# Optimization experiments

Measured on AMD Instinct MI355X. Metric: run time of the kernel, lower is better.

Reference implementation:

```python
import jax, jax.numpy as jnp
import numpy as np

BN_EPS = 1e-5


def setup_inputs() -> dict:
    key = jax.random.key(0)
    ks = jax.random.split(key, 6)
    B, C, N, K, T, O = 8, 64, 4096, 20, 3, 64
    feat = jax.random.normal(ks[0], (B, C, N), dtype=jnp.float32)
    idx = jax.random.randint(ks[1], (B, N, K), 0, N, dtype=jnp.int32)
    group_pc = jax.random.normal(ks[2], (B, 3, N, K), dtype=jnp.float32)
    weights = jax.random.normal(ks[3], (B, 20, T, N, K), dtype=jnp.float32) * 0.05
    conv_w = jax.random.normal(ks[4], (O, C * T, K), dtype=jnp.float32) * 0.02
    gamma = jnp.ones((O,), dtype=jnp.float32)
    beta = jnp.zeros((O,), dtype=jnp.float32)
    return {"feat": feat, "idx": idx, "group_pc": group_pc, "weights": weights,
            "conv_w": conv_w, "gamma": gamma, "beta": beta}


def _poly_terms(group_pc):
    # group_pc: (B, 3, N, K) -> 20 Taylor terms (B, 20, N, K)
    X, Y, Z = group_pc[:, 0], group_pc[:, 1], group_pc[:, 2]
    XX, YY, ZZ = X * X, Y * Y, Z * Z
    XY, XZ, YZ = X * Y, X * Z, Y * Z
    ones = jnp.ones_like(X)
    return jnp.stack([
        ones, X, Y, Z,
        XX, YY, ZZ,
        XX * X, YY * Y, ZZ * Z,
        XY, XZ, YZ,
        X * XY, X * XZ, Y * YZ, Y * XY, Z * XZ, Z * YZ, XY * Z,
    ], axis=1)


def reference(feat, idx, group_pc, weights, conv_w, gamma, beta):
    B, C, N = feat.shape
    K = idx.shape[-1]
    T = weights.shape[2]
    # KNN gather: group_feat[b, c, n, j] = feat[b, c, idx[b, n, j]]  -> (B, C, N, K)
    group_feat = jax.vmap(lambda f, i: f[:, i])(feat, idx)
    # 20 polynomial basis terms of XYZ: (B, 20, N, K)
    terms = _poly_terms(group_pc)
    # taylor[b, t, n, k] = sum_p weights[b, p, t, n, k] * terms[b, p, n, k]
    taylor = jnp.einsum('bptnk,bpnk->btnk', weights, terms)
    # Fused outer-product + [1, K] conv (output width 1, no bias since bn=True):
    # out[b, o, n] = sum_{c, t, k} group_feat[b,c,n,k] * taylor[b,t,n,k] * W[o, c*T+t, k]
    w = conv_w.reshape(conv_w.shape[0], C, T, K)
    out = jnp.einsum('bcnk,btnk,octk->bon', group_feat, taylor, w)
    # BatchNorm (training-mode batch stats over B and N) + ReLU
    mean = jnp.mean(out, axis=(0, 2), keepdims=True)
    var = jnp.var(out, axis=(0, 2), keepdims=True)
    out = gamma[None, :, None] * (out - mean) / jnp.sqrt(var + BN_EPS) + beta[None, :, None]
    return jax.nn.relu(out)
```

## Files before the change

kernel.cpp:

```cpp
#include <hip/hip_runtime.h>
#include <hip/hip_bf16.h>

#define B_ 8
#define C_ 64
#define N_ 4096
#define K_ 20
#define T_ 3
#define O_ 64
#define P_ 20
#define NK_ (N_ * K_)
#define BN_EPS 1e-5f
#define PADW 68

#define WS_FEATT 0
#define WS_WT (WS_FEATT + B_ * N_ * C_)
#define WS_TAY (WS_WT + 122880)
#define WS_RAW (WS_TAY + B_ * T_ * NK_)
#define WS_PART (WS_RAW + B_ * O_ * N_)
#define WS_STATS (WS_PART + 512 * O_ * 2)

typedef __attribute__((ext_vector_type(8))) short short8;
typedef __attribute__((ext_vector_type(16))) float f32x16;

__device__ inline unsigned cvtpk_bf16(float lo, float hi) {
    unsigned r;
    asm volatile("v_cvt_pk_bf16_f32 %0, %1, %2" : "=v"(r) : "v"(lo), "v"(hi));
    return r;
}

union U128 {
    uint4 u;
    short8 s;
};
__device__ inline short8 as_short8(uint4 u) {
    U128 x;
    x.u = u;
    return x.s;
}

__global__ void k_transpose_feat(const float* __restrict__ feat, float* __restrict__ featT) {
    __shared__ float t[64][65];
    int b = blockIdx.y;
    int n0 = blockIdx.x * 64;
    int lx = threadIdx.x & 63, ly = threadIdx.x >> 6;
    const float* fp = feat + b * C_ * N_;
#pragma unroll
    for (int cc = 0; cc < 16; ++cc) {
        int c = ly * 16 + cc;
        t[c][lx] = fp[c * N_ + n0 + lx];
    }
    __syncthreads();
    float* op = featT + (b * N_ + n0) * C_;
#pragma unroll
    for (int u = 0; u < 16; ++u) {
        int n = ly * 16 + u;
        op[n * C_ + lx] = t[lx][n];
    }
}

__global__ void k_pack_w(const float* __restrict__ cw, unsigned short* __restrict__ Wf) {
    int e = blockIdx.x * 256 + threadIdx.x;
    int j = e & 7;
    int l = (e >> 3) & 63;
    int frag = e >> 9;
    int oh = frag & 1;
    int cc = (frag >> 1) & 3;
    int kt = frag >> 3;
    int t = kt % 3, k = kt / 3;
    int o = oh * 32 + (l & 31);
    int c = cc * 16 + (l >> 5) * 8 + j;
    float v = cw[o * (C_ * T_ * K_) + (c * T_ + t) * K_ + k];
    Wf[e] = (unsigned short)(cvtpk_bf16(v, v) & 0xffffu);
}

__global__ void k_taylor(const float* __restrict__ W5, const float* __restrict__ gpc,
                         float* __restrict__ tay) {
    int tid = blockIdx.x * 256 + threadIdx.x;
    int b = tid / NK_;
    int nk = tid - b * NK_;
    const float X = gpc[b * 3 * NK_ + nk];
    const float Y = gpc[b * 3 * NK_ + NK_ + nk];
    const float Z = gpc[b * 3 * NK_ + 2 * NK_ + nk];
    float XX = X * X, YY = Y * Y, ZZ = Z * Z;
    float XY = X * Y, XZ = X * Z, YZ = Y * Z;
    float terms[20];
    terms[0] = 1.f; terms[1] = X;      terms[2] = Y;       terms[3] = Z;
    terms[4] = XX;  terms[5] = YY;     terms[6] = ZZ;
    terms[7] = XX * X; terms[8] = YY * Y; terms[9] = ZZ * Z;
    terms[10] = XY; terms[11] = XZ;    terms[12] = YZ;
    terms[13] = X * XY;
    terms[14] = X * XZ;
    terms[15] = Y * YZ;
    terms[16] = Y * XY;
    terms[17] = Z * XZ;
    terms[18] = Z * YZ;
    terms[19] = XY * Z;
    float a0 = 0.f, a1 = 0.f, a2 = 0.f;
    const float* wp = W5 + (size_t)b * P_ * T_ * NK_ + nk;
#pragma unroll
    for (int p = 0; p < P_; ++p) {
        float tp = terms[p];
        a0 += wp[0] * tp;
        a1 += wp[NK_] * tp;
        a2 += wp[2 * NK_] * tp;
        wp += 3 * NK_;
    }
    float* tp = tay + (size_t)b * T_ * NK_ + nk;
    tp[0] = a0;
    tp[NK_] = a1;
    tp[2 * NK_] = a2;
}

__global__ __launch_bounds__(512, 4) void k_main(const float* __restrict__ featT,
                                                 const unsigned short* __restrict__ Wf,
                                                 const float* __restrict__ tay,
                                                 const int* __restrict__ idx,
                                                 float* __restrict__ raw,
                                                 float* __restrict__ part) {
    __shared__ float G[2][64][PADW];
    __shared__ union {
        struct {
            float tayS[3][K_][64];
            int idxS[K_][64];
        } s;
        float out[64][68];
    } su;

    const int bid0 = blockIdx.x;
    const int bid = (bid0 & 7) * 64 + (bid0 >> 3);
    const int b = bid >> 6;
    const int n0 = (bid & 63) << 6;
    const int tid = threadIdx.x;
    const int lane = tid & 63;
    const int wv = tid >> 6;
    const int wc = wv & 3;
    const int wo = wv >> 2;
    const int nl = lane & 31;
    const int kf = lane >> 5;

    {
        const int* ip = idx + (b * N_ + n0) * K_;
        for (int e = tid; e < 64 * K_; e += 512) su.s.idxS[e % K_][e / K_] = ip[e];
#pragma unroll
        for (int t = 0; t < 3; ++t) {
            const float* tp = tay + ((size_t)(b * 3 + t) * N_ + n0) * K_;
            for (int e = tid; e < 64 * K_; e += 512) su.s.tayS[t][e % K_][e / K_] = tp[e];
        }
    }
    __syncthreads();

    f32x16 acc[2];
#pragma unroll
    for (int nh = 0; nh < 2; ++nh)
#pragma unroll
        for (int i = 0; i < 16; ++i) acc[nh][i] = 0.f;

    const float* fb = featT + (size_t)b * N_ * C_;
    const int r1 = tid >> 4, r2 = r1 + 32, sseg = tid & 15;

    float4 st1 = *(const float4*)(fb + su.s.idxS[0][r1] * C_ + sseg * 4);
    float4 st2 = *(const float4*)(fb + su.s.idxS[0][r2] * C_ + sseg * 4);

    for (int k = 0; k < K_; ++k) {
        float* Gb = &G[k & 1][0][0];
        *(float4*)(Gb + r1 * PADW + sseg * 4) = st1;
        *(float4*)(Gb + r2 * PADW + sseg * 4) = st2;
        __syncthreads();
        if (k + 1 < K_) {
            st1 = *(const float4*)(fb + su.s.idxS[k + 1][r1] * C_ + sseg * 4);
            st2 = *(const float4*)(fb + su.s.idxS[k + 1][r2] * C_ + sseg * 4);
        }
        const float* row0 = Gb + nl * PADW + wc * 16 + kf * 8;
        const float* row1 = Gb + (nl + 32) * PADW + wc * 16 + kf * 8;
        float4 u0 = *(const float4*)row0, u1 = *(const float4*)(row0 + 4);
        float4 w0 = *(const float4*)row1, w1 = *(const float4*)(row1 + 4);
        float g0[8] = {u0.x, u0.y, u0.z, u0.w, u1.x, u1.y, u1.z, u1.w};
        float g1[8] = {w0.x, w0.y, w0.z, w0.w, w1.x, w1.y, w1.z, w1.w};
#pragma unroll
        for (int t = 0; t < 3; ++t) {
            uint4 ar = *(const uint4*)(Wf +
                                       (size_t)((((k * 3 + t) * 4 + wc) * 2 + wo) * 64 + lane) * 8);
            float tv0 = su.s.tayS[t][k][nl];
            float tv1 = su.s.tayS[t][k][nl + 32];
            unsigned p0[4], p1[4];
#pragma unroll
            for (int p = 0; p < 4; ++p) {
                p0[p] = cvtpk_bf16(g0[2 * p] * tv0, g0[2 * p + 1] * tv0);
                p1[p] = cvtpk_bf16(g1[2 * p] * tv1, g1[2 * p + 1] * tv1);
            }
            short8 bf0 = as_short8(make_uint4(p0[0], p0[1], p0[2], p0[3]));
            short8 bf1 = as_short8(make_uint4(p1[0], p1[1], p1[2], p1[3]));
            short8 a0 = as_short8(ar);
            acc[0] = __builtin_amdgcn_mfma_f32_32x32x16_bf16(a0, bf0, acc[0], 0, 0, 0);
            acc[1] = __builtin_amdgcn_mfma_f32_32x32x16_bf16(a0, bf1, acc[1], 0, 0, 0);
        }
    }

    __syncthreads();
#pragma unroll 1
    for (int ww = 0; ww < 4; ++ww) {
        if (wc == ww) {
#pragma unroll
            for (int nh = 0; nh < 2; ++nh)
#pragma unroll
                for (int r = 0; r < 16; ++r) {
                    int row = wo * 32 + (r & 3) + ((r >> 2) << 3) + (kf << 2);
                    int col = nh * 32 + nl;
                    if (ww == 0)
                        su.out[row][col] = acc[nh][r];
                    else
                        su.out[row][col] += acc[nh][r];
                }
        }
        __syncthreads();
    }

    if (tid < 256) {
        int o = tid >> 2, seg = tid & 3;
        float4* dst = (float4*)(raw + ((b * O_ + o) * N_) + n0 + seg * 16);
        const float* srow = &su.out[o][seg * 16];
        dst[0] = *(const float4*)&srow[0];
        dst[1] = *(const float4*)&srow[4];
        dst[2] = *(const float4*)&srow[8];
        dst[3] = *(const float4*)&srow[12];
    }
    if (tid < 64) {
        float s1 = 0.f, s2 = 0.f;
#pragma unroll 8
        for (int n = 0; n < 64; ++n) {
            float v = su.out[tid][n];
            s1 += v;
            s2 += v * v;
        }
        part[(bid * 64 + tid) * 2 + 0] = s1;
        part[(bid * 64 + tid) * 2 + 1] = s2;
    }
}

__global__ void k_bnstats(const float* __restrict__ part, const float* __restrict__ gamma,
                          const float* __restrict__ beta, float* __restrict__ stats) {
    int o = blockIdx.x;
    int tid = threadIdx.x;
    __shared__ float s1s[256], s2s[256];
    float s1 = 0.f, s2 = 0.f;
    for (int j = tid; j < 512; j += 256) {
        s1 += part[(j * 64 + o) * 2 + 0];
        s2 += part[(j * 64 + o) * 2 + 1];
    }
    s1s[tid] = s1;
    s2s[tid] = s2;
    __syncthreads();
    for (int s = 128; s > 0; s >>= 1) {
        if (tid < s) {
            s1s[tid] += s1s[tid + s];
            s2s[tid] += s2s[tid + s];
        }
        __syncthreads();
    }
    if (tid == 0) {
        const float cnt = (float)(B_ * N_);
        float mean = s1s[0] / cnt;
        float var = s2s[0] / cnt - mean * mean;
        float sc = gamma[o] * rsqrtf(var + BN_EPS);
        stats[o * 2 + 0] = sc;
        stats[o * 2 + 1] = beta[o] - mean * sc;
    }
}

__global__ void k_finalize(const float* __restrict__ raw, const float* __restrict__ stats,
                           float* __restrict__ out) {
    int e = (blockIdx.x * 256 + threadIdx.x) * 4;
    int o = (e >> 12) & 63;
    float sc = stats[o * 2 + 0], sh = stats[o * 2 + 1];
    float4 v = *(const float4*)(raw + e);
    v.x = fmaxf(v.x * sc + sh, 0.f);
    v.y = fmaxf(v.y * sc + sh, 0.f);
    v.z = fmaxf(v.z * sc + sh, 0.f);
    v.w = fmaxf(v.w * sc + sh, 0.f);
    *(float4*)(out + e) = v;
}

extern "C" void kernel_launch(void* const* d_in, const int* in_sizes, int n_in,
                              void* d_out, int out_size, void* d_ws, size_t ws_size,
                              hipStream_t stream) {
    const float* feat = (const float*)d_in[0];
    const int* idx = (const int*)d_in[1];
    const float* gpc = (const float*)d_in[2];
    const float* weights = (const float*)d_in[3];
    const float* conv_w = (const float*)d_in[4];
    const float* gamma = (const float*)d_in[5];
    const float* beta = (const float*)d_in[6];
    float* out = (float*)d_out;
    float* ws = (float*)d_ws;

    float* featT = ws + WS_FEATT;
    unsigned short* Wf = (unsigned short*)(ws + WS_WT);
    float* tay = ws + WS_TAY;
    float* raw = ws + WS_RAW;
    float* part = ws + WS_PART;
    float* stats = ws + WS_STATS;

    hipLaunchKernelGGL(k_transpose_feat, dim3(N_ / 64, B_), dim3(256), 0, stream, feat, featT);
    hipLaunchKernelGGL(k_pack_w, dim3((K_ * T_ * C_ * O_) / 256), dim3(256), 0, stream, conv_w,
                       Wf);
    hipLaunchKernelGGL(k_taylor, dim3(B_ * NK_ / 256), dim3(256), 0, stream, weights, gpc, tay);
    hipLaunchKernelGGL(k_main, dim3(B_ * (N_ / 64)), dim3(512), 0, stream, featT, Wf, tay, idx,
                       raw, part);
    hipLaunchKernelGGL(k_bnstats, dim3(O_), dim3(256), 0, stream, part, gamma, beta, stats);
    hipLaunchKernelGGL(k_finalize, dim3(B_ * O_ * N_ / 4 / 256), dim3(256), 0, stream, raw, stats,
                       out);
}
```

Measured before the change: 83.65 us.

## Fuse Taylor weighting into main kernel and switch MFMA path to fp16

```diff
diff --git a/kernel.cpp b/kernel.cpp
--- a/kernel.cpp
+++ b/kernel.cpp
@@ -14,34 +14,42 @@
 
 #define WS_FEATT 0
 #define WS_WT (WS_FEATT + B_ * N_ * C_)
-#define WS_TAY (WS_WT + 122880)
-#define WS_RAW (WS_TAY + B_ * T_ * NK_)
+#define WS_RAW (WS_WT + 122880)
 #define WS_PART (WS_RAW + B_ * O_ * N_)
 #define WS_STATS (WS_PART + 512 * O_ * 2)
 
-typedef __attribute__((ext_vector_type(8))) short short8;
+typedef __attribute__((ext_vector_type(8))) _Float16 half8;
+typedef __attribute__((ext_vector_type(2))) _Float16 half2v;
+typedef __attribute__((ext_vector_type(2))) __fp16 fp16x2;
 typedef __attribute__((ext_vector_type(16))) float f32x16;
 
-__device__ inline unsigned cvtpk_bf16(float lo, float hi) {
-    unsigned r;
-    asm volatile("v_cvt_pk_bf16_f32 %0, %1, %2" : "=v"(r) : "v"(lo), "v"(hi));
-    return r;
-}
-
-union U128 {
+union UH8 {
     uint4 u;
-    short8 s;
+    half8 h;
+    half2v h2[4];
 };
-__device__ inline short8 as_short8(uint4 u) {
-    U128 x;
-    x.u = u;
-    return x.s;
+union UH2 {
+    unsigned u;
+    half2v h;
+    fp16x2 f;
+};
+
+__device__ inline half2v cvt_pkrtz(float a, float b) {
+    UH2 x;
+    x.f = __builtin_amdgcn_cvt_pkrtz(a, b);
+    return x.h;
+}
+__device__ inline unsigned cvt_pkrtz_u(float a, float b) {
+    UH2 x;
+    x.f = __builtin_amdgcn_cvt_pkrtz(a, b);
+    return x.u;
 }
 
 __global__ void k_transpose_feat(const float* __restrict__ feat, float* __restrict__ featT) {
     __shared__ float t[64][65];
-    int b = blockIdx.y;
-    int n0 = blockIdx.x * 64;
+    int bid = blockIdx.x;
+    int b = bid & 7;
+    int n0 = (bid >> 3) << 6;
     int lx = threadIdx.x & 63, ly = threadIdx.x >> 6;
     const float* fp = feat + b * C_ * N_;
 #pragma unroll
@@ -58,7 +66,7 @@
     }
 }
 
-__global__ void k_pack_w(const float* __restrict__ cw, unsigned short* __restrict__ Wf) {
+__global__ void k_pack_w(const float* __restrict__ cw, _Float16* __restrict__ Wh) {
     int e = blockIdx.x * 256 + threadIdx.x;
     int j = e & 7;
     int l = (e >> 3) & 63;
@@ -69,58 +77,20 @@
     int t = kt % 3, k = kt / 3;
     int o = oh * 32 + (l & 31);
     int c = cc * 16 + (l >> 5) * 8 + j;
-    float v = cw[o * (C_ * T_ * K_) + (c * T_ + t) * K_ + k];
-    Wf[e] = (unsigned short)(cvtpk_bf16(v, v) & 0xffffu);
-}
-
-__global__ void k_taylor(const float* __restrict__ W5, const float* __restrict__ gpc,
-                         float* __restrict__ tay) {
-    int tid = blockIdx.x * 256 + threadIdx.x;
-    int b = tid / NK_;
-    int nk = tid - b * NK_;
-    const float X = gpc[b * 3 * NK_ + nk];
-    const float Y = gpc[b * 3 * NK_ + NK_ + nk];
-    const float Z = gpc[b * 3 * NK_ + 2 * NK_ + nk];
-    float XX = X * X, YY = Y * Y, ZZ = Z * Z;
-    float XY = X * Y, XZ = X * Z, YZ = Y * Z;
-    float terms[20];
-    terms[0] = 1.f; terms[1] = X;      terms[2] = Y;       terms[3] = Z;
-    terms[4] = XX;  terms[5] = YY;     terms[6] = ZZ;
-    terms[7] = XX * X; terms[8] = YY * Y; terms[9] = ZZ * Z;
-    terms[10] = XY; terms[11] = XZ;    terms[12] = YZ;
-    terms[13] = X * XY;
-    terms[14] = X * XZ;
-    terms[15] = Y * YZ;
-    terms[16] = Y * XY;
-    terms[17] = Z * XZ;
-    terms[18] = Z * YZ;
-    terms[19] = XY * Z;
-    float a0 = 0.f, a1 = 0.f, a2 = 0.f;
-    const float* wp = W5 + (size_t)b * P_ * T_ * NK_ + nk;
-#pragma unroll
-    for (int p = 0; p < P_; ++p) {
-        float tp = terms[p];
-        a0 += wp[0] * tp;
-        a1 += wp[NK_] * tp;
-        a2 += wp[2 * NK_] * tp;
-        wp += 3 * NK_;
-    }
-    float* tp = tay + (size_t)b * T_ * NK_ + nk;
-    tp[0] = a0;
-    tp[NK_] = a1;
-    tp[2 * NK_] = a2;
+    Wh[e] = (_Float16)cw[o * (C_ * T_ * K_) + (c * T_ + t) * K_ + k];
 }
 
 __global__ __launch_bounds__(512, 4) void k_main(const float* __restrict__ featT,
-                                                 const unsigned short* __restrict__ Wf,
-                                                 const float* __restrict__ tay,
+                                                 const _Float16* __restrict__ Wh,
+                                                 const float* __restrict__ weights,
+                                                 const float* __restrict__ gpc,
                                                  const int* __restrict__ idx,
                                                  float* __restrict__ raw,
                                                  float* __restrict__ part) {
     __shared__ float G[2][64][PADW];
     __shared__ union {
         struct {
-            float tayS[3][K_][64];
+            unsigned tayH[3][K_][64];
             int idxS[K_][64];
         } s;
         float out[64][68];
@@ -141,10 +111,42 @@
     {
         const int* ip = idx + (b * N_ + n0) * K_;
         for (int e = tid; e < 64 * K_; e += 512) su.s.idxS[e % K_][e / K_] = ip[e];
-#pragma unroll
-        for (int t = 0; t < 3; ++t) {
-            const float* tp = tay + ((size_t)(b * 3 + t) * N_ + n0) * K_;
-            for (int e = tid; e < 64 * K_; e += 512) su.s.tayS[t][e % K_][e / K_] = tp[e];
+    }
+    {
+        const float* gpcb = gpc + (size_t)b * 3 * NK_ + n0 * K_;
+        const float* wb = weights + (size_t)b * P_ * T_ * NK_ + n0 * K_;
+        for (int e = tid; e < 64 * K_; e += 512) {
+            float X = gpcb[e];
+            float Y = gpcb[NK_ + e];
+            float Z = gpcb[2 * NK_ + e];
+            float XX = X * X, YY = Y * Y, ZZ = Z * Z;
+            float XY = X * Y, XZ = X * Z, YZ = Y * Z;
+            float terms[20];
+            terms[0] = 1.f; terms[1] = X;      terms[2] = Y;       terms[3] = Z;
+            terms[4] = XX;  terms[5] = YY;     terms[6] = ZZ;
+            terms[7] = XX * X; terms[8] = YY * Y; terms[9] = ZZ * Z;
+            terms[10] = XY; terms[11] = XZ;    terms[12] = YZ;
+            terms[13] = X * XY;
+            terms[14] = X * XZ;
+            terms[15] = Y * YZ;
+            terms[16] = Y * XY;
+            terms[17] = Z * XZ;
+            terms[18] = Z * YZ;
+            terms[19] = XY * Z;
+            float a0 = 0.f, a1 = 0.f, a2 = 0.f;
+            const float* wp = wb + e;
+#pragma unroll
+            for (int p = 0; p < P_; ++p) {
+                float tp = terms[p];
+                a0 += wp[0] * tp;
+                a1 += wp[NK_] * tp;
+                a2 += wp[2 * NK_] * tp;
+                wp += 3 * NK_;
+            }
+            int n = e / K_, k = e - n * K_;
+            su.s.tayH[0][k][n] = cvt_pkrtz_u(a0, a0);
+            su.s.tayH[1][k][n] = cvt_pkrtz_u(a1, a1);
+            su.s.tayH[2][k][n] = cvt_pkrtz_u(a2, a2);
         }
     }
     __syncthreads();
@@ -174,25 +176,31 @@
         const float* row1 = Gb + (nl + 32) * PADW + wc * 16 + kf * 8;
         float4 u0 = *(const float4*)row0, u1 = *(const float4*)(row0 + 4);
         float4 w0 = *(const float4*)row1, w1 = *(const float4*)(row1 + 4);
-        float g0[8] = {u0.x, u0.y, u0.z, u0.w, u1.x, u1.y, u1.z, u1.w};
-        float g1[8] = {w0.x, w0.y, w0.z, w0.w, w1.x, w1.y, w1.z, w1.w};
+        half2v h0[4], h1[4];
+        h0[0] = cvt_pkrtz(u0.x, u0.y);
+        h0[1] = cvt_pkrtz(u0.z, u0.w);
+        h0[2] = cvt_pkrtz(u1.x, u1.y);
+        h0[3] = cvt_pkrtz(u1.z, u1.w);
+        h1[0] = cvt_pkrtz(w0.x, w0.y);
+        h1[1] = cvt_pkrtz(w0.z, w0.w);
+        h1[2] = cvt_pkrtz(w1.x, w1.y);
+        h1[3] = cvt_pkrtz(w1.z, w1.w);
 #pragma unroll
         for (int t = 0; t < 3; ++t) {
-            uint4 ar = *(const uint4*)(Wf +
-                                       (size_t)((((k * 3 + t) * 4 + wc) * 2 + wo) * 64 + lane) * 8);
-            float tv0 = su.s.tayS[t][k][nl];
-            float tv1 = su.s.tayS[t][k][nl + 32];
-            unsigned p0[4], p1[4];
-#pragma unroll
-            for (int p = 0; p < 4; ++p) {
-                p0[p] = cvtpk_bf16(g0[2 * p] * tv0, g0[2 * p + 1] * tv0);
-                p1[p] = cvtpk_bf16(g1[2 * p] * tv1, g1[2 * p + 1] * tv1);
+            UH8 ar;
+            ar.u = *(const uint4*)(Wh +
+                                   (size_t)((((k * 3 + t) * 4 + wc) * 2 + wo) * 64 + lane) * 8);
+            UH2 tv0, tv1;
+            tv0.u = su.s.tayH[t][k][nl];
+            tv1.u = su.s.tayH[t][k][nl + 32];
+            UH8 b0, b1;
+#pragma unroll
+            for (int i = 0; i < 4; ++i) {
+                b0.h2[i] = h0[i] * tv0.h;
+                b1.h2[i] = h1[i] * tv1.h;
             }
-            short8 bf0 = as_short8(make_uint4(p0[0], p0[1], p0[2], p0[3]));
-            short8 bf1 = as_short8(make_uint4(p1[0], p1[1], p1[2], p1[3]));
-            short8 a0 = as_short8(ar);
-            acc[0] = __builtin_amdgcn_mfma_f32_32x32x16_bf16(a0, bf0, acc[0], 0, 0, 0);
-            acc[1] = __builtin_amdgcn_mfma_f32_32x32x16_bf16(a0, bf1, acc[1], 0, 0, 0);
+            acc[0] = __builtin_amdgcn_mfma_f32_32x32x16_f16(ar.h, b0.h, acc[0], 0, 0, 0);
+            acc[1] = __builtin_amdgcn_mfma_f32_32x32x16_f16(ar.h, b1.h, acc[1], 0, 0, 0);
         }
     }
 
@@ -294,18 +302,16 @@
     float* ws = (float*)d_ws;
 
     float* featT = ws + WS_FEATT;
-    unsigned short* Wf = (unsigned short*)(ws + WS_WT);
-    float* tay = ws + WS_TAY;
+    _Float16* Wh = (_Float16*)(ws + WS_WT);
     float* raw = ws + WS_RAW;
     float* part = ws + WS_PART;
     float* stats = ws + WS_STATS;
 
-    hipLaunchKernelGGL(k_transpose_feat, dim3(N_ / 64, B_), dim3(256), 0, stream, feat, featT);
+    hipLaunchKernelGGL(k_transpose_feat, dim3(512), dim3(256), 0, stream, feat, featT);
     hipLaunchKernelGGL(k_pack_w, dim3((K_ * T_ * C_ * O_) / 256), dim3(256), 0, stream, conv_w,
-                       Wf);
-    hipLaunchKernelGGL(k_taylor, dim3(B_ * NK_ / 256), dim3(256), 0, stream, weights, gpc, tay);
-    hipLaunchKernelGGL(k_main, dim3(B_ * (N_ / 64)), dim3(512), 0, stream, featT, Wf, tay, idx,
-                       raw, part);
+                       Wh);
+    hipLaunchKernelGGL(k_main, dim3(B_ * (N_ / 64)), dim3(512), 0, stream, featT, Wh, weights,
+                       gpc, idx, raw, part);
     hipLaunchKernelGGL(k_bnstats, dim3(O_), dim3(256), 0, stream, part, gamma, beta, stats);
     hipLaunchKernelGGL(k_finalize, dim3(B_ * O_ * N_ / 4 / 256), dim3(256), 0, stream, raw, stats,
                        out);
```

After: 74.60 us. -10.8%, faster.
